# Optimization experiments

Hardware: AMD Instinct MI355X
Metric: run time of the kernel (lower is better)

## Reference

```python
import jax, jax.numpy as jnp
import numpy as np

B, D_IN, H = 16384, 512, 1024


def setup_inputs() -> dict:
    key = jax.random.key(0)
    ks = jax.random.split(key, 12)
    s_in = 1.0 / np.sqrt(D_IN)
    s_h = 1.0 / np.sqrt(H)
    d = {
        "input_x": jax.random.normal(ks[0], (B, D_IN), jnp.float32),
        "h_old": jax.random.normal(ks[1], (B, H), jnp.float32),
        "c_old": jax.random.normal(ks[2], (B, H), jnp.float32),
    }
    names_U = ["Ui", "Uf", "Uo", "Uc"]
    names_W = ["Wi", "Wf", "Wo", "Wc"]
    for i, n in enumerate(names_U):
        d[n + "_w"] = jax.random.normal(ks[3 + i], (D_IN, H), jnp.float32) * s_in
        d[n + "_b"] = jnp.zeros((H,), jnp.float32)
    for i, n in enumerate(names_W):
        d[n + "_w"] = jax.random.normal(ks[7 + i], (H, H), jnp.float32) * s_h
        d[n + "_b"] = jnp.zeros((H,), jnp.float32)
    return d


def reference(input_x, h_old, c_old,
              Ui_w, Ui_b, Wi_w, Wi_b,
              Uf_w, Uf_b, Wf_w, Wf_b,
              Uo_w, Uo_b, Wo_w, Wo_b,
              Uc_w, Uc_b, Wc_w, Wc_b):
    # Fuse the 8 small GEMMs into 2: concatenate gate projections along the
    # output dim (math identical to 8 separate Dense layers + adds).
    U = jnp.concatenate([Ui_w, Uf_w, Uo_w, Uc_w], axis=1)   # [D_in, 4H]
    W = jnp.concatenate([Wi_w, Wf_w, Wo_w, Wc_w], axis=1)   # [H, 4H]
    b = jnp.concatenate([Ui_b + Wi_b, Uf_b + Wf_b, Uo_b + Wo_b, Uc_b + Wc_b])
    gates = input_x @ U + h_old @ W + b                      # [B, 4H]
    i_t, f_t, o_t, g_t = jnp.split(gates, 4, axis=1)
    i_t = jax.nn.sigmoid(i_t)
    f_t = jax.nn.sigmoid(f_t)
    o_t = jax.nn.sigmoid(o_t)
    c_t = jnp.tanh(g_t)
    c = i_t * c_t + f_t * c_old
    h_new = o_t * jnp.tanh(c)
    return (h_new, c)
```

## Files before the change

kernel.cpp:

```cpp
#include <hip/hip_runtime.h>
#include <hip/hip_bf16.h>
#include <stdint.h>

#define B_ROWS 16384
#define D_IN   512
#define H_DIM  1024
#define K_TOT  1536
#define NT64   24

typedef __attribute__((ext_vector_type(8)))  short bf16x8;
typedef __attribute__((ext_vector_type(4)))  float f32x4;
typedef __attribute__((ext_vector_type(4)))  float float4v;
typedef __attribute__((ext_vector_type(8)))  unsigned short u16x8;

__device__ __forceinline__ unsigned short f2bf(float f) {
    uint32_t u = __float_as_uint(f);
    u = (u + 0x7FFFu + ((u >> 16) & 1u)) >> 16;
    return (unsigned short)u;
}

__global__ void cvt_A(const float* __restrict__ x, const float* __restrict__ h,
                      unsigned short* __restrict__ Ag) {
    int t     = blockIdx.x * blockDim.x + threadIdx.x;
    int lane  = t & 63;
    int chunk = (t >> 6) & 15;
    int kh    = (t >> 10) & 1;
    int rest  = t >> 11;
    int T     = rest % 24;
    int bm    = rest / 24;
    int row   = bm * 256 + chunk * 16 + (lane & 15);
    int k     = T * 64 + kh * 32 + (lane >> 4) * 8;
    const float* src = (k < 512) ? (x + (size_t)row * D_IN + k)
                                 : (h + (size_t)row * H_DIM + (k - 512));
    float4v v0 = *(const float4v*)(src);
    float4v v1 = *(const float4v*)(src + 4);
    u16x8 o;
    o[0] = f2bf(v0[0]); o[1] = f2bf(v0[1]); o[2] = f2bf(v0[2]); o[3] = f2bf(v0[3]);
    o[4] = f2bf(v1[0]); o[5] = f2bf(v1[1]); o[6] = f2bf(v1[2]); o[7] = f2bf(v1[3]);
    *(u16x8*)(Ag + (size_t)t * 8) = o;
}

__global__ void cvt_B(const float* __restrict__ Ui, const float* __restrict__ Uf,
                      const float* __restrict__ Uo, const float* __restrict__ Uc,
                      const float* __restrict__ Wi, const float* __restrict__ Wf,
                      const float* __restrict__ Wo, const float* __restrict__ Wc,
                      unsigned short* __restrict__ Bg) {
    int t     = blockIdx.x * blockDim.x + threadIdx.x;
    int lane  = t & 63;
    int chunk = (t >> 6) & 15;
    int kh    = (t >> 10) & 1;
    int rest  = t >> 11;
    int T     = rest % 24;
    int bn    = rest / 24;
    int c     = bn * 256 + chunk * 16 + (lane & 15);
    int g     = (c >> 4) & 3;
    int hcol  = ((c >> 6) << 4) | (c & 15);
    int k     = T * 64 + kh * 32 + (lane >> 4) * 8;
    const float* up = (g == 0) ? Ui : (g == 1) ? Uf : (g == 2) ? Uo : Uc;
    const float* wp = (g == 0) ? Wi : (g == 1) ? Wf : (g == 2) ? Wo : Wc;
    u16x8 o;
    if (k < 512) {
        const float* s = up + (size_t)k * H_DIM + hcol;
        #pragma unroll
        for (int i = 0; i < 8; ++i) o[i] = f2bf(s[(size_t)i * H_DIM]);
    } else {
        const float* s = wp + (size_t)(k - 512) * H_DIM + hcol;
        #pragma unroll
        for (int i = 0; i < 8; ++i) o[i] = f2bf(s[(size_t)i * H_DIM]);
    }
    *(u16x8*)(Bg + (size_t)t * 8) = o;
}

__global__ void cvt_bias(const float* __restrict__ Uib, const float* __restrict__ Ufb,
                         const float* __restrict__ Uob, const float* __restrict__ Ucb,
                         const float* __restrict__ Wib, const float* __restrict__ Wfb,
                         const float* __restrict__ Wob, const float* __restrict__ Wcb,
                         float* __restrict__ bias) {
    int t = blockIdx.x * blockDim.x + threadIdx.x;
    int g = t >> 10, h = t & 1023;
    const float* ub = (g == 0) ? Uib : (g == 1) ? Ufb : (g == 2) ? Uob : Ucb;
    const float* wb = (g == 0) ? Wib : (g == 1) ? Wfb : (g == 2) ? Wob : Wcb;
    bias[t] = ub[h] + wb[h];
}

__global__ __launch_bounds__(512) void lstm_gemm(
        const unsigned short* __restrict__ Ag, const unsigned short* __restrict__ Bg,
        const float* __restrict__ bias, const float* __restrict__ c_old,
        float* __restrict__ out) {
    __shared__ __align__(1024) char lds[131072];

    const int tid = threadIdx.x;
    const int l   = tid & 63;
    const int wv  = tid >> 6;
    const int wm  = wv >> 2;
    const int wn  = wv & 3;

    const int orig = blockIdx.x;
    const int xcd  = orig & 7;
    const int jj   = orig >> 3;
    const int bn   = (xcd & 3) * 4 + (jj & 3);
    const int bm   = (xcd >> 2) * 32 + (jj >> 2);

    const unsigned short* aSrc = Ag + (size_t)bm * 24 * 16384 + tid * 8;
    const unsigned short* bSrc = Bg + (size_t)bn * 24 * 16384 + tid * 8;

    const int aRd = wm * 8192 + l * 16;
    const int bRd = wn * 4096 + l * 16;

#define GLDS(SRC, DST) __builtin_amdgcn_global_load_lds(                            \
        (const __attribute__((address_space(1))) void*)(SRC),                       \
        (__attribute__((address_space(3))) void*)(DST), 16, 0, 0)

#define STAGE(MAT, T, KH, BUF) do {                                                 \
    const unsigned short* _s = ((MAT) ? bSrc : aSrc) + (size_t)((T) * 2 + (KH)) * 8192; \
    char* _d = (char*)lds + (BUF) * 65536 + (MAT) * 32768 + (KH) * 16384 + wv * 1024;   \
    GLDS(_s, _d);  GLDS(_s + 4096, _d + 8192);                                      \
} while (0)

    f32x4 acc[8][4] = {};
    bf16x8 bPers[4];

#define PHASE(BUF, KH, Q, RB, SM, ST, SKH, SBUF, GATE) do {                         \
    const char* _Ab = (const char*)lds + (BUF) * 65536 + (KH) * 16384 + aRd;        \
    bf16x8 aF[4];                                                                   \
    _Pragma("unroll") for (int m = 0; m < 4; ++m)                                   \
        aF[m] = *(const bf16x8*)(_Ab + ((Q) * 4 + m) * 1024);                       \
    if (RB) {                                                                       \
        const char* _Bb = (const char*)lds + (BUF) * 65536 + 32768 + (KH) * 16384 + bRd; \
        _Pragma("unroll") for (int n = 0; n < 4; ++n)                               \
            bPers[n] = *(const bf16x8*)(_Bb + n * 1024);                            \
    }                                                                               \
    STAGE(SM, ST, SKH, SBUF);                                                       \
    __builtin_amdgcn_s_barrier();                                                   \
    asm volatile("s_waitcnt lgkmcnt(0)" ::: "memory");                              \
    __builtin_amdgcn_sched_barrier(0);                                              \
    __builtin_amdgcn_s_setprio(1);                                                  \
    _Pragma("unroll") for (int m = 0; m < 4; ++m)                                   \
        _Pragma("unroll") for (int n = 0; n < 4; ++n)                               \
            acc[(Q) * 4 + m][n] = __builtin_amdgcn_mfma_f32_16x16x32_bf16(          \
                aF[m], bPers[n], acc[(Q) * 4 + m][n], 0, 0, 0);                     \
    __builtin_amdgcn_s_setprio(0);                                                  \
    if (GATE) { asm volatile("s_waitcnt vmcnt(4)\ns_barrier" ::: "memory"); }       \
    else      { asm volatile("s_barrier" ::: "memory"); }                           \
} while (0)

    STAGE(0, 0, 0, 0); STAGE(1, 0, 0, 0);
    STAGE(0, 0, 1, 0); STAGE(1, 0, 1, 0);
    STAGE(0, 1, 0, 1); STAGE(1, 1, 0, 1);
    asm volatile("s_waitcnt vmcnt(4)\ns_barrier" ::: "memory");

    #pragma unroll 1
    for (int i = 0; i < 12; ++i) {
        const int t1 = 2 * i + 1;
        int t2 = 2 * i + 2; if (t2 >= NT64) t2 -= NT64;
        int t3 = 2 * i + 3; if (t3 >= NT64) t3 -= NT64;
        PHASE(0, 0, 0, 1,  0, t1, 1, 1,  0);
        PHASE(0, 0, 1, 0,  1, t1, 1, 1,  0);
        PHASE(0, 1, 0, 1,  0, t2, 0, 0,  0);
        PHASE(0, 1, 1, 0,  1, t2, 0, 0,  1);
        PHASE(1, 0, 0, 1,  0, t2, 1, 0,  0);
        PHASE(1, 0, 1, 0,  1, t2, 1, 0,  0);
        PHASE(1, 1, 0, 1,  0, t3, 0, 1,  0);
        PHASE(1, 1, 1, 0,  1, t3, 0, 1,  1);
    }
    asm volatile("s_waitcnt vmcnt(0)" ::: "memory");

    const int hh  = (bn * 4 + wn) * 16 + (l & 15);
    const float bi  = bias[hh];
    const float bff = bias[1024 + hh];
    const float bo  = bias[2048 + hh];
    const float bc  = bias[3072 + hh];

    #pragma unroll
    for (int a = 0; a < 8; ++a) {
        const int rb = bm * 256 + wm * 128 + (a >> 2) * 64 + (a & 3) * 16 + ((l >> 4) * 4);
        #pragma unroll
        for (int j = 0; j < 4; ++j) {
            const int r = rb + j;
            float iv = acc[a][0][j] + bi;
            float fv = acc[a][1][j] + bff;
            float ov = acc[a][2][j] + bo;
            float gv = acc[a][3][j] + bc;
            float it = 1.f / (1.f + __expf(-iv));
            float ft = 1.f / (1.f + __expf(-fv));
            float ot = 1.f / (1.f + __expf(-ov));
            float gt = 1.f - 2.f / (1.f + __expf(2.f * gv));
            float co = c_old[(size_t)r * H_DIM + hh];
            float cn = it * gt + ft * co;
            float th = 1.f - 2.f / (1.f + __expf(2.f * cn));
            out[(size_t)r * H_DIM + hh] = ot * th;
            out[(size_t)B_ROWS * H_DIM + (size_t)r * H_DIM + hh] = cn;
        }
    }
#undef PHASE
#undef STAGE
#undef GLDS
}

extern "C" void kernel_launch(void* const* d_in, const int* in_sizes, int n_in,
                              void* d_out, int out_size, void* d_ws, size_t ws_size,
                              hipStream_t stream) {
    const float* x  = (const float*)d_in[0];
    const float* h0 = (const float*)d_in[1];
    const float* c0 = (const float*)d_in[2];
    const float* Uw[4] = {(const float*)d_in[3],  (const float*)d_in[5],
                          (const float*)d_in[7],  (const float*)d_in[9]};
    const float* Ub[4] = {(const float*)d_in[4],  (const float*)d_in[6],
                          (const float*)d_in[8],  (const float*)d_in[10]};
    const float* Ww[4] = {(const float*)d_in[11], (const float*)d_in[13],
                          (const float*)d_in[15], (const float*)d_in[17]};
    const float* Wb[4] = {(const float*)d_in[12], (const float*)d_in[14],
                          (const float*)d_in[16], (const float*)d_in[18]};

    unsigned short* Ag = (unsigned short*)d_ws;
    unsigned short* Bg = Ag + (size_t)B_ROWS * K_TOT;
    float* bias        = (float*)(Bg + (size_t)4096 * K_TOT);
    float* out         = (float*)d_out;

    cvt_A<<<12288, 256, 0, stream>>>(x, h0, Ag);
    cvt_B<<<3072, 256, 0, stream>>>(Uw[0], Uw[1], Uw[2], Uw[3],
                                    Ww[0], Ww[1], Ww[2], Ww[3], Bg);
    cvt_bias<<<16, 256, 0, stream>>>(Ub[0], Ub[1], Ub[2], Ub[3],
                                     Wb[0], Wb[1], Wb[2], Wb[3], bias);
    lstm_gemm<<<1024, 512, 0, stream>>>(Ag, Bg, bias, c0, out);
}
```

Baseline: 256.7 us.

## Restructure GEMM pipeline into five-slot ring of 32-wide K tiles

The GEMM main loop now walks 48 K-tiles of width 32 instead of 24 tiles of width 64 split into halves. Each tile goes into a 5-slot LDS ring (160 KB), with loads issued three tiles ahead. The A/B pre-conversion kernels change their packed layout to match. The goal is deeper prefetch and simpler, more regular phases, so memory latency hides better behind MFMA work. The cost is more LDS, which rules out a second block per CU, and more barriers per unit of compute.

```diff
diff --git a/kernel.cpp b/kernel.cpp
--- a/kernel.cpp
+++ b/kernel.cpp
@@ -6,7 +6,7 @@
 #define D_IN   512
 #define H_DIM  1024
 #define K_TOT  1536
-#define NT64   24
+#define NKT    48
 
 typedef __attribute__((ext_vector_type(8)))  short bf16x8;
 typedef __attribute__((ext_vector_type(4)))  float f32x4;
@@ -24,12 +24,11 @@
     int t     = blockIdx.x * blockDim.x + threadIdx.x;
     int lane  = t & 63;
     int chunk = (t >> 6) & 15;
-    int kh    = (t >> 10) & 1;
-    int rest  = t >> 11;
-    int T     = rest % 24;
-    int bm    = rest / 24;
+    int rest  = t >> 10;
+    int T     = rest % 48;
+    int bm    = rest / 48;
     int row   = bm * 256 + chunk * 16 + (lane & 15);
-    int k     = T * 64 + kh * 32 + (lane >> 4) * 8;
+    int k     = T * 32 + (lane >> 4) * 8;
     const float* src = (k < 512) ? (x + (size_t)row * D_IN + k)
                                  : (h + (size_t)row * H_DIM + (k - 512));
     float4v v0 = *(const float4v*)(src);
@@ -48,14 +47,13 @@
     int t     = blockIdx.x * blockDim.x + threadIdx.x;
     int lane  = t & 63;
     int chunk = (t >> 6) & 15;
-    int kh    = (t >> 10) & 1;
-    int rest  = t >> 11;
-    int T     = rest % 24;
-    int bn    = rest / 24;
+    int rest  = t >> 10;
+    int T     = rest % 48;
+    int bn    = rest / 48;
     int c     = bn * 256 + chunk * 16 + (lane & 15);
     int g     = (c >> 4) & 3;
     int hcol  = ((c >> 6) << 4) | (c & 15);
-    int k     = T * 64 + kh * 32 + (lane >> 4) * 8;
+    int k     = T * 32 + (lane >> 4) * 8;
     const float* up = (g == 0) ? Ui : (g == 1) ? Uf : (g == 2) ? Uo : Uc;
     const float* wp = (g == 0) ? Wi : (g == 1) ? Wf : (g == 2) ? Wo : Wc;
     u16x8 o;
@@ -87,7 +85,7 @@
         const unsigned short* __restrict__ Ag, const unsigned short* __restrict__ Bg,
         const float* __restrict__ bias, const float* __restrict__ c_old,
         float* __restrict__ out) {
-    __shared__ __align__(1024) char lds[131072];
+    __shared__ __align__(1024) char lds[163840];
 
     const int tid = threadIdx.x;
     const int l   = tid & 63;
@@ -101,69 +99,90 @@
     const int bn   = (xcd & 3) * 4 + (jj & 3);
     const int bm   = (xcd >> 2) * 32 + (jj >> 2);
 
-    const unsigned short* aSrc = Ag + (size_t)bm * 24 * 16384 + tid * 8;
-    const unsigned short* bSrc = Bg + (size_t)bn * 24 * 16384 + tid * 8;
+    const unsigned short* aSrc = Ag + (size_t)bm * 48 * 8192 + (size_t)(2 * wv) * 512 + l * 8;
+    const unsigned short* bSrc = Bg + (size_t)bn * 48 * 8192 + (size_t)(2 * wv) * 512 + l * 8;
 
     const int aRd = wm * 8192 + l * 16;
-    const int bRd = wn * 4096 + l * 16;
+    const int bRd = 16384 + wn * 4096 + l * 16;
 
 #define GLDS(SRC, DST) __builtin_amdgcn_global_load_lds(                            \
         (const __attribute__((address_space(1))) void*)(SRC),                       \
         (__attribute__((address_space(3))) void*)(DST), 16, 0, 0)
 
-#define STAGE(MAT, T, KH, BUF) do {                                                 \
-    const unsigned short* _s = ((MAT) ? bSrc : aSrc) + (size_t)((T) * 2 + (KH)) * 8192; \
-    char* _d = (char*)lds + (BUF) * 65536 + (MAT) * 32768 + (KH) * 16384 + wv * 1024;   \
-    GLDS(_s, _d);  GLDS(_s + 4096, _d + 8192);                                      \
+#define STAGE_A(T, SLOTBASE) do {                                                   \
+    const unsigned short* _s = aSrc + (size_t)(T) * 8192;                           \
+    char* _d = (char*)lds + (SLOTBASE) + wv * 2048;                                 \
+    GLDS(_s, _d);  GLDS(_s + 512, _d + 1024);                                       \
+} while (0)
+
+#define STAGE_B(T, SLOTBASE) do {                                                   \
+    const unsigned short* _s = bSrc + (size_t)(T) * 8192;                           \
+    char* _d = (char*)lds + (SLOTBASE) + 16384 + wv * 2048;                         \
+    GLDS(_s, _d);  GLDS(_s + 512, _d + 1024);                                       \
 } while (0)
 
     f32x4 acc[8][4] = {};
     bf16x8 bPers[4];
 
-#define PHASE(BUF, KH, Q, RB, SM, ST, SKH, SBUF, GATE) do {                         \
-    const char* _Ab = (const char*)lds + (BUF) * 65536 + (KH) * 16384 + aRd;        \
-    bf16x8 aF[4];                                                                   \
-    _Pragma("unroll") for (int m = 0; m < 4; ++m)                                   \
-        aF[m] = *(const bf16x8*)(_Ab + ((Q) * 4 + m) * 1024);                       \
-    if (RB) {                                                                       \
-        const char* _Bb = (const char*)lds + (BUF) * 65536 + 32768 + (KH) * 16384 + bRd; \
-        _Pragma("unroll") for (int n = 0; n < 4; ++n)                               \
-            bPers[n] = *(const bf16x8*)(_Bb + n * 1024);                            \
-    }                                                                               \
-    STAGE(SM, ST, SKH, SBUF);                                                       \
-    __builtin_amdgcn_s_barrier();                                                   \
-    asm volatile("s_waitcnt lgkmcnt(0)" ::: "memory");                              \
-    __builtin_amdgcn_sched_barrier(0);                                              \
-    __builtin_amdgcn_s_setprio(1);                                                  \
-    _Pragma("unroll") for (int m = 0; m < 4; ++m)                                   \
-        _Pragma("unroll") for (int n = 0; n < 4; ++n)                               \
-            acc[(Q) * 4 + m][n] = __builtin_amdgcn_mfma_f32_16x16x32_bf16(          \
-                aF[m], bPers[n], acc[(Q) * 4 + m][n], 0, 0, 0);                     \
-    __builtin_amdgcn_s_setprio(0);                                                  \
-    if (GATE) { asm volatile("s_waitcnt vmcnt(4)\ns_barrier" ::: "memory"); }       \
-    else      { asm volatile("s_barrier" ::: "memory"); }                           \
-} while (0)
-
-    STAGE(0, 0, 0, 0); STAGE(1, 0, 0, 0);
-    STAGE(0, 0, 1, 0); STAGE(1, 0, 1, 0);
-    STAGE(0, 1, 0, 1); STAGE(1, 1, 0, 1);
-    asm volatile("s_waitcnt vmcnt(4)\ns_barrier" ::: "memory");
+    STAGE_A(0, 0);      STAGE_B(0, 0);
+    STAGE_A(1, 32768);  STAGE_B(1, 32768);
+    STAGE_A(2, 65536);  STAGE_B(2, 65536);
+    asm volatile("s_waitcnt vmcnt(2)");
+    __builtin_amdgcn_s_barrier();
+
+    int rdBase = 0;
+    int ssBase = 98304;
 
     #pragma unroll 1
-    for (int i = 0; i < 12; ++i) {
-        const int t1 = 2 * i + 1;
-        int t2 = 2 * i + 2; if (t2 >= NT64) t2 -= NT64;
-        int t3 = 2 * i + 3; if (t3 >= NT64) t3 -= NT64;
-        PHASE(0, 0, 0, 1,  0, t1, 1, 1,  0);
-        PHASE(0, 0, 1, 0,  1, t1, 1, 1,  0);
-        PHASE(0, 1, 0, 1,  0, t2, 0, 0,  0);
-        PHASE(0, 1, 1, 0,  1, t2, 0, 0,  1);
-        PHASE(1, 0, 0, 1,  0, t2, 1, 0,  0);
-        PHASE(1, 0, 1, 0,  1, t2, 1, 0,  0);
-        PHASE(1, 1, 0, 1,  0, t3, 0, 1,  0);
-        PHASE(1, 1, 1, 0,  1, t3, 0, 1,  1);
+    for (int t = 0; t < NKT; ++t) {
+        int ts = t + 3; if (ts >= NKT) ts -= NKT;
+
+        {
+            const char* _A = (const char*)lds + rdBase + aRd;
+            const char* _B = (const char*)lds + rdBase + bRd;
+            bf16x8 aF[4];
+            #pragma unroll
+            for (int m = 0; m < 4; ++m)
+                aF[m] = *(const bf16x8*)(_A + m * 1024);
+            #pragma unroll
+            for (int n = 0; n < 4; ++n)
+                bPers[n] = *(const bf16x8*)(_B + n * 1024);
+            STAGE_A(ts, ssBase);
+            __builtin_amdgcn_s_barrier();
+            __builtin_amdgcn_s_setprio(1);
+            #pragma unroll
+            for (int m = 0; m < 4; ++m)
+                #pragma unroll
+                for (int n = 0; n < 4; ++n)
+                    acc[m][n] = __builtin_amdgcn_mfma_f32_16x16x32_bf16(
+                        aF[m], bPers[n], acc[m][n], 0, 0, 0);
+            __builtin_amdgcn_s_setprio(0);
+            __builtin_amdgcn_s_barrier();
+        }
+        {
+            const char* _A = (const char*)lds + rdBase + aRd + 4096;
+            bf16x8 aF[4];
+            #pragma unroll
+            for (int m = 0; m < 4; ++m)
+                aF[m] = *(const bf16x8*)(_A + m * 1024);
+            STAGE_B(ts, ssBase);
+            __builtin_amdgcn_s_barrier();
+            __builtin_amdgcn_s_setprio(1);
+            #pragma unroll
+            for (int m = 0; m < 4; ++m)
+                #pragma unroll
+                for (int n = 0; n < 4; ++n)
+                    acc[4 + m][n] = __builtin_amdgcn_mfma_f32_16x16x32_bf16(
+                        aF[m], bPers[n], acc[4 + m][n], 0, 0, 0);
+            __builtin_amdgcn_s_setprio(0);
+            asm volatile("s_waitcnt vmcnt(2)");
+            __builtin_amdgcn_s_barrier();
+        }
+
+        rdBase = (rdBase == 131072) ? 0 : rdBase + 32768;
+        ssBase = (ssBase == 131072) ? 0 : ssBase + 32768;
     }
-    asm volatile("s_waitcnt vmcnt(0)" ::: "memory");
+    asm volatile("s_waitcnt vmcnt(0)");
 
     const int hh  = (bn * 4 + wn) * 16 + (l & 15);
     const float bi  = bias[hh];
@@ -192,8 +211,8 @@
             out[(size_t)B_ROWS * H_DIM + (size_t)r * H_DIM + hh] = cn;
         }
     }
-#undef PHASE
-#undef STAGE
+#undef STAGE_A
+#undef STAGE_B
 #undef GLDS
 }
 
```

Result: slower. 265.5 us (+3.4%).
